# Optimization experiments

Hardware: AMD Instinct MI355X
Metric: run time of the kernel (lower is better)

The kernel has to match this reference:

```python
import jax, jax.numpy as jnp
import numpy as np
from jax import lax

T_LEN, BATCH, D_IN, D_HID, N_LAYERS = 512, 32, 512, 512, 4


def setup_inputs() -> dict:
    key = jax.random.key(0)
    kx, kw, ku = jax.random.split(key, 3)
    x = jax.random.normal(kx, (T_LEN, BATCH, D_IN), dtype=jnp.float32)
    # xavier-ish scale on input kernels to keep the relu recurrence stable
    W = jax.random.normal(kw, (N_LAYERS, D_HID, D_IN), dtype=jnp.float32) * (1.0 / np.sqrt(D_IN))
    b = jnp.zeros((N_LAYERS, D_HID), dtype=jnp.float32)
    # diagonal recurrent weights in [0,1) so |u|<=1 (non-exploding)
    u = jax.random.uniform(ku, (N_LAYERS, D_HID), dtype=jnp.float32)
    return {"x": x, "W": W, "b": b, "u": u}


def _indrnn_layer(x, W_l, b_l, u_l):
    # x: [T, B, Din]; precompute input projection as one big GEMM
    xh = jnp.einsum('tbd,hd->tbh', x, W_l) + b_l  # [T, B, Dh]
    h0 = jnp.zeros((x.shape[1], W_l.shape[0]), dtype=x.dtype)

    def step(h, xh_t):
        h_new = jax.nn.relu(xh_t + u_l * h)
        return h_new, h_new

    _, outs = lax.scan(step, h0, xh)
    return outs  # [T, B, Dh]


def reference(x, W, b, u):
    out = x
    for l in range(W.shape[0]):  # fixed small layer count
        out = _indrnn_layer(out, W[l], b[l], u[l])
    return out
```

## Files before the change

kernel.cpp:

```cpp
#include <hip/hip_runtime.h>
#include <hip/hip_bf16.h>

typedef short bf16x8 __attribute__((ext_vector_type(8)));
typedef float f32x4 __attribute__((ext_vector_type(4)));

#define T_LEN 512
#define BATCH 32
#define D 512
#define M_TOT (T_LEN * BATCH)
#define NLAYER 4

#define BM 128
#define BN 128
#define BK 64
#define NT (D / BK)
#define EP 72

#define RBM 128
#define RBN 64
#define RSLOT (RBM * BK + RBN * BK)
#define RSMEM_BYTES (3 * RSLOT * 2)
#define REP 40

#define CH 32
#define NCH (T_LEN / CH)

#define SBAR()                             \
    do {                                   \
        __builtin_amdgcn_s_barrier();      \
        __builtin_amdgcn_sched_barrier(0); \
    } while (0)
#define VMCNT(n)                                                   \
    do {                                                           \
        asm volatile("s_waitcnt vmcnt(" #n ")" ::: "memory");      \
        __builtin_amdgcn_sched_barrier(0);                         \
    } while (0)

__global__ __launch_bounds__(256) void convert_k(const float* __restrict__ W,
                                                 __hip_bfloat16* __restrict__ Wb) {
    const int i = (blockIdx.x * 256 + threadIdx.x) * 4;
    float4 v = *(const float4*)(W + i);
    __hip_bfloat16 h0 = __float2bfloat16(v.x);
    __hip_bfloat16 h1 = __float2bfloat16(v.y);
    __hip_bfloat16 h2 = __float2bfloat16(v.z);
    __hip_bfloat16 h3 = __float2bfloat16(v.w);
    ushort4 o;
    o.x = *(const unsigned short*)&h0;
    o.y = *(const unsigned short*)&h1;
    o.z = *(const unsigned short*)&h2;
    o.w = *(const unsigned short*)&h3;
    *(ushort4*)(Wb + i) = o;
}

__global__ __launch_bounds__(256) void gemm_l0(const float* __restrict__ Agf0,
                                               const __hip_bfloat16* __restrict__ Bt,
                                               const float* __restrict__ bias,
                                               __hip_bfloat16* __restrict__ Cb) {
    constexpr int K = D;
    constexpr int N = D;
    __shared__ __hip_bfloat16 smem[4 * BM * BK];
    __hip_bfloat16* const AsP[2] = {smem, smem + BM * BK};
    __hip_bfloat16* const BsP[2] = {smem + 2 * BM * BK, smem + 3 * BM * BK};

    const int tid  = threadIdx.x;
    const int wave = tid >> 6;
    const int lane = tid & 63;

    const int bid = blockIdx.x;
    const int xcd = bid & 7;
    const int jb  = bid >> 3;
    const int bm  = xcd * 16 + (jb >> 2);
    const int bn  = jb & 3;

    const int wm = (wave >> 1) * 64;
    const int wn = (wave & 1) * 64;

    const int srow = lane >> 3;
    const int scol = ((lane & 7) ^ srow) * 8;

    const float* Agf = Agf0 + (size_t)(bm * BM) * K;
    const __hip_bfloat16* Bg = Bt + (size_t)(bn * BN) * K;

    f32x4 acc[4][4] = {};
    float4 va[4][2];

#define STAGE_B0(buf, k0)                                                                            \
    do {                                                                                             \
        _Pragma("unroll") for (int jj = 0; jj < 4; ++jj) {                                           \
            const int rbase = (jj * 4 + wave) * 8;                                                   \
            __builtin_amdgcn_global_load_lds(                                                        \
                (const __attribute__((address_space(1))) void*)(Bg + (size_t)(rbase + srow) * K + (k0) + scol), \
                (__attribute__((address_space(3))) void*)(&BsP[buf][rbase * BK]), 16, 0, 0);         \
        }                                                                                            \
    } while (0)

#define LOAD_A0(k0)                                                                                  \
    do {                                                                                             \
        _Pragma("unroll") for (int jj = 0; jj < 4; ++jj) {                                           \
            const int rbase = (jj * 4 + wave) * 8;                                                   \
            const float* s = Agf + (size_t)(rbase + srow) * K + (k0) + scol;                         \
            va[jj][0] = *(const float4*)s;                                                           \
            va[jj][1] = *(const float4*)(s + 4);                                                     \
        }                                                                                            \
    } while (0)

#define WRITE_A0(buf)                                                                                \
    do {                                                                                             \
        _Pragma("unroll") for (int jj = 0; jj < 4; ++jj) {                                           \
            const int rbase = (jj * 4 + wave) * 8;                                                   \
            bf16x8 pk;                                                                               \
            _Pragma("unroll") for (int q = 0; q < 4; ++q) {                                          \
                __hip_bfloat16 t0 = __float2bfloat16(((const float*)&va[jj][0])[q]);                 \
                __hip_bfloat16 t1 = __float2bfloat16(((const float*)&va[jj][1])[q]);                 \
                pk[q]     = *(const short*)&t0;                                                      \
                pk[q + 4] = *(const short*)&t1;                                                      \
            }                                                                                        \
            *(bf16x8*)(&AsP[buf][(rbase + srow) * BK + (lane & 7) * 8]) = pk;                        \
        }                                                                                            \
    } while (0)

#define COMPUTE0(buf)                                                                                \
    do {                                                                                             \
        bf16x8 af[4][2], bv[4][2];                                                                   \
        const int fr = lane & 15;                                                                    \
        const int kq = lane >> 4;                                                                    \
        _Pragma("unroll") for (int mi = 0; mi < 4; ++mi) {                                           \
            const int r = wm + mi * 16 + fr;                                                         \
            _Pragma("unroll") for (int kh = 0; kh < 2; ++kh) {                                       \
                const int c = ((kh * 4 + kq) ^ (fr & 7)) * 8;                                        \
                af[mi][kh] = *(const bf16x8*)(&AsP[buf][r * BK + c]);                                \
            }                                                                                        \
        }                                                                                            \
        _Pragma("unroll") for (int ni = 0; ni < 4; ++ni) {                                           \
            const int r = wn + ni * 16 + fr;                                                         \
            _Pragma("unroll") for (int kh = 0; kh < 2; ++kh) {                                       \
                const int c = ((kh * 4 + kq) ^ (fr & 7)) * 8;                                        \
                bv[ni][kh] = *(const bf16x8*)(&BsP[buf][r * BK + c]);                                \
            }                                                                                        \
        }                                                                                            \
        _Pragma("unroll") for (int kh = 0; kh < 2; ++kh)                                             \
            _Pragma("unroll") for (int mi = 0; mi < 4; ++mi)                                         \
                _Pragma("unroll") for (int ni = 0; ni < 4; ++ni)                                     \
                    acc[mi][ni] = __builtin_amdgcn_mfma_f32_16x16x32_bf16(af[mi][kh], bv[ni][kh],    \
                                                                          acc[mi][ni], 0, 0, 0);    \
    } while (0)

    LOAD_A0(0);
    STAGE_B0(0, 0);
    WRITE_A0(0);
    __syncthreads();
    int cur = 0;
#pragma unroll
    for (int kt = 1; kt < NT; ++kt) {
        LOAD_A0(kt * BK);
        STAGE_B0(cur ^ 1, kt * BK);
        COMPUTE0(cur);
        WRITE_A0(cur ^ 1);
        __syncthreads();
        cur ^= 1;
    }
    COMPUTE0(cur);
    __syncthreads();

    {
        __hip_bfloat16* S = smem + wave * (64 * EP);
        const int cfr = lane & 15;
        const int cfq = lane >> 4;
        float bs[4];
#pragma unroll
        for (int ni = 0; ni < 4; ++ni) bs[ni] = bias[bn * BN + wn + ni * 16 + cfr];
#pragma unroll
        for (int mi = 0; mi < 4; ++mi)
#pragma unroll
            for (int ni = 0; ni < 4; ++ni)
#pragma unroll
                for (int r = 0; r < 4; ++r)
                    S[(mi * 16 + cfq * 4 + r) * EP + ni * 16 + cfr] =
                        __float2bfloat16(acc[mi][ni][r] + bs[ni]);
        const int rq = lane >> 3;
        const int cl = (lane & 7) * 8;
#pragma unroll
        for (int p = 0; p < 8; ++p) {
            const int lr = p * 8 + rq;
            bf16x8 v = *(const bf16x8*)(S + lr * EP + cl);
            *(bf16x8*)(&Cb[(size_t)(bm * BM + wm + lr) * N + bn * BN + wn + cl]) = v;
        }
    }
#undef STAGE_B0
#undef LOAD_A0
#undef WRITE_A0
#undef COMPUTE0
}

__global__ __launch_bounds__(256) void gemm_r3(const __hip_bfloat16* __restrict__ A,
                                               const __hip_bfloat16* __restrict__ Bt,
                                               const float* __restrict__ bias,
                                               __hip_bfloat16* __restrict__ Cb) {
    constexpr int K = D;
    constexpr int N = D;
    extern __shared__ __hip_bfloat16 smem[];

    const int tid  = threadIdx.x;
    const int wave = tid >> 6;
    const int lane = tid & 63;

    const int bid = blockIdx.x;
    const int xcd = bid & 7;
    const int jb  = bid >> 3;
    const int bm  = xcd * 16 + (jb >> 3);
    const int bn  = jb & 7;

    const int wm = (wave >> 1) * 64;
    const int wn = (wave & 1) * 32;

    const int srow = lane >> 3;
    const int scol = ((lane & 7) ^ srow) * 8;

    const __hip_bfloat16* Ag = A  + (size_t)(bm * RBM) * K;
    const __hip_bfloat16* Bg = Bt + (size_t)(bn * RBN) * K;

    f32x4 acc[4][2] = {};

#define STAGE(slot, k0)                                                                              \
    do {                                                                                             \
        __hip_bfloat16* const Asl = smem + (slot) * RSLOT;                                           \
        __hip_bfloat16* const Bsl = Asl + RBM * BK;                                                  \
        _Pragma("unroll") for (int jj = 0; jj < 4; ++jj) {                                           \
            const int rbase = (wave * 4 + jj) * 8;                                                   \
            __builtin_amdgcn_global_load_lds(                                                        \
                (const __attribute__((address_space(1))) void*)(Ag + (size_t)(rbase + srow) * K + (k0) + scol), \
                (__attribute__((address_space(3))) void*)(Asl + rbase * BK), 16, 0, 0);              \
        }                                                                                            \
        _Pragma("unroll") for (int jj = 0; jj < 2; ++jj) {                                           \
            const int rbase = (wave * 2 + jj) * 8;                                                   \
            __builtin_amdgcn_global_load_lds(                                                        \
                (const __attribute__((address_space(1))) void*)(Bg + (size_t)(rbase + srow) * K + (k0) + scol), \
                (__attribute__((address_space(3))) void*)(Bsl + rbase * BK), 16, 0, 0);              \
        }                                                                                            \
    } while (0)

#define COMPUTE(slot)                                                                                \
    do {                                                                                             \
        const __hip_bfloat16* const Asl = smem + (slot) * RSLOT;                                     \
        const __hip_bfloat16* const Bsl = Asl + RBM * BK;                                            \
        bf16x8 af[4][2], bv[2][2];                                                                   \
        const int fr = lane & 15;                                                                    \
        const int kq = lane >> 4;                                                                    \
        _Pragma("unroll") for (int mi = 0; mi < 4; ++mi) {                                           \
            const int r = wm + mi * 16 + fr;                                                         \
            _Pragma("unroll") for (int kh = 0; kh < 2; ++kh) {                                       \
                const int c = ((kh * 4 + kq) ^ (fr & 7)) * 8;                                        \
                af[mi][kh] = *(const bf16x8*)(&Asl[r * BK + c]);                                     \
            }                                                                                        \
        }                                                                                            \
        _Pragma("unroll") for (int ni = 0; ni < 2; ++ni) {                                           \
            const int r = wn + ni * 16 + fr;                                                         \
            _Pragma("unroll") for (int kh = 0; kh < 2; ++kh) {                                       \
                const int c = ((kh * 4 + kq) ^ (fr & 7)) * 8;                                        \
                bv[ni][kh] = *(const bf16x8*)(&Bsl[r * BK + c]);                                     \
            }                                                                                        \
        }                                                                                            \
        _Pragma("unroll") for (int kh = 0; kh < 2; ++kh)                                             \
            _Pragma("unroll") for (int mi = 0; mi < 4; ++mi)                                         \
                _Pragma("unroll") for (int ni = 0; ni < 2; ++ni)                                     \
                    acc[mi][ni] = __builtin_amdgcn_mfma_f32_16x16x32_bf16(af[mi][kh], bv[ni][kh],    \
                                                                          acc[mi][ni], 0, 0, 0);    \
    } while (0)

    STAGE(0, 0);
    STAGE(1, BK);
    VMCNT(6);
    SBAR();

#pragma unroll
    for (int t = 0; t < NT; ++t) {
        if (t + 2 < NT) STAGE((t + 2) % 3, (t + 2) * BK);
        COMPUTE(t % 3);
        if (t < NT - 1) {
            if (t + 2 < NT) {
                VMCNT(6);
            } else {
                VMCNT(0);
            }
            SBAR();
        }
    }
    __syncthreads();

    {
        __hip_bfloat16* S = smem + wave * (64 * REP);
        const int cfr = lane & 15;
        const int cfq = lane >> 4;
        float bs[2];
#pragma unroll
        for (int ni = 0; ni < 2; ++ni) bs[ni] = bias[bn * RBN + wn + ni * 16 + cfr];
#pragma unroll
        for (int mi = 0; mi < 4; ++mi)
#pragma unroll
            for (int ni = 0; ni < 2; ++ni)
#pragma unroll
                for (int r = 0; r < 4; ++r)
                    S[(mi * 16 + cfq * 4 + r) * REP + ni * 16 + cfr] =
                        __float2bfloat16(acc[mi][ni][r] + bs[ni]);
        const int rq = lane >> 2;
        const int cl = (lane & 3) * 8;
#pragma unroll
        for (int p = 0; p < 4; ++p) {
            const int lr = p * 16 + rq;
            bf16x8 v = *(const bf16x8*)(S + lr * REP + cl);
            *(bf16x8*)(&Cb[(size_t)(bm * RBM + wm + lr) * N + bn * RBN + wn + cl]) = v;
        }
    }
#undef STAGE
#undef COMPUTE
}

template <int MODE>
__global__ __launch_bounds__(512) void scan_k(const __hip_bfloat16* __restrict__ xh,
                                              const float* __restrict__ u,
                                              float* __restrict__ outf,
                                              __hip_bfloat16* __restrict__ outb) {
    __shared__ float4 md[NCH][32];
    const int i2  = threadIdx.x & 31;
    const int c   = threadIdx.x >> 5;
    const int idx = blockIdx.x * 64 + i2 * 2;
    const float u0 = u[idx & (D - 1)];
    const float u1 = u[(idx + 1) & (D - 1)];

    const __hip_bfloat16* p = xh + (size_t)c * CH * M_TOT + idx;
    unsigned int xv[CH];
#pragma unroll
    for (int t = 0; t < CH; ++t) xv[t] = *(const unsigned int*)(p + (size_t)t * M_TOT);

    float m0 = 0.f, d0 = 0.f, m1 = 0.f, d1 = 0.f;
#pragma unroll
    for (int t = 0; t < CH; ++t) {
        const float a0 = __uint_as_float(xv[t] << 16);
        const float a1 = __uint_as_float(xv[t] & 0xffff0000u);
        m0 = fmaxf(fmaf(u0, m0, a0), 0.f);
        d0 = fmaf(u0, d0, a0);
        m1 = fmaxf(fmaf(u1, m1, a1), 0.f);
        d1 = fmaf(u1, d1, a1);
    }
    md[c][i2] = make_float4(m0, d0, m1, d1);
    __syncthreads();

    float e0 = u0 * u0, e1 = u1 * u1;
    e0 *= e0; e0 *= e0; e0 *= e0; e0 *= e0;
    e1 *= e1; e1 *= e1; e1 *= e1; e1 *= e1;
    float h0 = 0.f, h1 = 0.f;
    for (int jj = 0; jj < c; ++jj) {
        const float4 v = md[jj][i2];
        h0 = fmaxf(v.x, fmaf(e0, h0, v.y));
        h1 = fmaxf(v.z, fmaf(e1, h1, v.w));
    }

    const size_t base = (size_t)c * CH * M_TOT + idx;
#pragma unroll
    for (int t = 0; t < CH; ++t) {
        const size_t off = base + (size_t)t * M_TOT;
        const float a0 = __uint_as_float(xv[t] << 16);
        const float a1 = __uint_as_float(xv[t] & 0xffff0000u);
        h0 = fmaxf(fmaf(u0, h0, a0), 0.f);
        h1 = fmaxf(fmaf(u1, h1, a1), 0.f);
        if (MODE & 1) *(float2*)(outf + off) = make_float2(h0, h1);
        if (MODE & 2) {
            __hip_bfloat16 b0 = __float2bfloat16(h0);
            __hip_bfloat16 b1 = __float2bfloat16(h1);
            unsigned int pk = (unsigned int)(*(unsigned short*)&b0) |
                              ((unsigned int)(*(unsigned short*)&b1) << 16);
            *(unsigned int*)(outb + off) = pk;
        }
    }
}

extern "C" void kernel_launch(void* const* d_in, const int* in_sizes, int n_in,
                              void* d_out, int out_size, void* d_ws, size_t ws_size,
                              hipStream_t stream) {
    const float* x = (const float*)d_in[0];
    const float* W = (const float*)d_in[1];
    const float* b = (const float*)d_in[2];
    const float* u = (const float*)d_in[3];
    float* out = (float*)d_out;

    __hip_bfloat16* Wb = (__hip_bfloat16*)d_ws;
    __hip_bfloat16* Ab = (__hip_bfloat16*)((char*)d_ws + (size_t)NLAYER * D * D * 2);
    __hip_bfloat16* Xh = Ab + (size_t)M_TOT * D;

    (void)hipFuncSetAttribute((const void*)gemm_r3,
                              hipFuncAttributeMaxDynamicSharedMemorySize, RSMEM_BYTES);

    convert_k<<<(NLAYER * D * D / 4) / 256, 256, 0, stream>>>(W, Wb);

    for (int l = 0; l < NLAYER; ++l) {
        if (l == 0) {
            gemm_l0<<<(M_TOT / BM) * (D / BN), 256, 0, stream>>>(x, Wb, b, Xh);
        } else {
            gemm_r3<<<(M_TOT / RBM) * (D / RBN), 256, RSMEM_BYTES, stream>>>(
                Ab, Wb + (size_t)l * D * D, b + (size_t)l * D, Xh);
        }
        if (l < NLAYER - 1) {
            scan_k<2><<<M_TOT / 64, 512, 0, stream>>>(Xh, u + (size_t)l * D, nullptr, Ab);
        } else {
            scan_k<1><<<M_TOT / 64, 512, 0, stream>>>(Xh, u + (size_t)l * D, out, nullptr);
        }
    }
}
```

Baseline: 116.2 us.

## Keep the weight tile resident in LDS with per-wave streamed A tiles

Replaces the 128x64 triple-buffered GEMM used for layers 1-3 with a 256x64-tile, 512-thread kernel. The block loads its full 64xK weight slice into LDS once. Each of the 8 waves then streams its own 32-row activation slice through a private double buffer, so the K-loop needs no block-wide barriers and sets MFMA priority around the math. The aim is to cut repeated weight loads and barrier stalls, at the cost of higher LDS use per block and lower occupancy.

```diff
diff --git a/kernel.cpp b/kernel.cpp
--- a/kernel.cpp
+++ b/kernel.cpp
@@ -16,11 +16,13 @@
 #define NT (D / BK)
 #define EP 72
 
-#define RBM 128
-#define RBN 64
-#define RSLOT (RBM * BK + RBN * BK)
-#define RSMEM_BYTES (3 * RSLOT * 2)
-#define REP 40
+#define QBN 64
+#define QWROWS 32
+#define QBM 256
+#define QB_ELEMS (QBN * D)
+#define QA_SLOT (QWROWS * BK)
+#define QSMEM_BYTES ((QB_ELEMS + 8 * 2 * QA_SLOT) * 2)
+#define QEP 72
 
 #define CH 32
 #define NCH (T_LEN / CH)
@@ -30,10 +32,15 @@
         __builtin_amdgcn_s_barrier();      \
         __builtin_amdgcn_sched_barrier(0); \
     } while (0)
-#define VMCNT(n)                                                   \
-    do {                                                           \
-        asm volatile("s_waitcnt vmcnt(" #n ")" ::: "memory");      \
-        __builtin_amdgcn_sched_barrier(0);                         \
+#define VMCNT(n)                                              \
+    do {                                                      \
+        asm volatile("s_waitcnt vmcnt(" #n ")" ::: "memory"); \
+        __builtin_amdgcn_sched_barrier(0);                    \
+    } while (0)
+#define LGKM0()                                               \
+    do {                                                      \
+        asm volatile("s_waitcnt lgkmcnt(0)" ::: "memory");    \
+        __builtin_amdgcn_sched_barrier(0);                    \
     } while (0)
 
 __global__ __launch_bounds__(256) void convert_k(const float* __restrict__ W,
@@ -192,10 +199,10 @@
 #undef COMPUTE0
 }
 
-__global__ __launch_bounds__(256) void gemm_r3(const __hip_bfloat16* __restrict__ A,
-                                               const __hip_bfloat16* __restrict__ Bt,
-                                               const float* __restrict__ bias,
-                                               __hip_bfloat16* __restrict__ Cb) {
+__global__ __launch_bounds__(512) void gemm_resB(const __hip_bfloat16* __restrict__ A,
+                                                 const __hip_bfloat16* __restrict__ Bt,
+                                                 const float* __restrict__ bias,
+                                                 __hip_bfloat16* __restrict__ Cb) {
     constexpr int K = D;
     constexpr int N = D;
     extern __shared__ __hip_bfloat16 smem[];
@@ -207,112 +214,112 @@
     const int bid = blockIdx.x;
     const int xcd = bid & 7;
     const int jb  = bid >> 3;
-    const int bm  = xcd * 16 + (jb >> 3);
+    const int bm  = xcd * 8 + (jb >> 3);
     const int bn  = jb & 7;
 
-    const int wm = (wave >> 1) * 64;
-    const int wn = (wave & 1) * 32;
+    __hip_bfloat16* const Bsm = smem;
+    __hip_bfloat16* const Awv = smem + QB_ELEMS + wave * (2 * QA_SLOT);
 
     const int srow = lane >> 3;
-    const int scol = ((lane & 7) ^ srow) * 8;
-
-    const __hip_bfloat16* Ag = A  + (size_t)(bm * RBM) * K;
-    const __hip_bfloat16* Bg = Bt + (size_t)(bn * RBN) * K;
-
-    f32x4 acc[4][2] = {};
-
-#define STAGE(slot, k0)                                                                              \
+    const int sch  = lane & 7;
+
+    const __hip_bfloat16* Agw = A + (size_t)(bm * QBM + wave * QWROWS) * K;
+    const __hip_bfloat16* Bg  = Bt + (size_t)(bn * QBN) * K;
+
+    f32x4 acc[2][4] = {};
+
+#pragma unroll
+    for (int p = 0; p < 8; ++p) {
+        const int row = p * 8 + wave;
+        const int sc  = ((lane & ~7) | ((lane & 7) ^ (row & 7))) * 8;
+        __builtin_amdgcn_global_load_lds(
+            (const __attribute__((address_space(1))) void*)(Bg + (size_t)row * K + sc),
+            (__attribute__((address_space(3))) void*)(Bsm + row * D), 16, 0, 0);
+    }
+#define STAGE_A(slot, k0)                                                                            \
     do {                                                                                             \
-        __hip_bfloat16* const Asl = smem + (slot) * RSLOT;                                           \
-        __hip_bfloat16* const Bsl = Asl + RBM * BK;                                                  \
         _Pragma("unroll") for (int jj = 0; jj < 4; ++jj) {                                           \
-            const int rbase = (wave * 4 + jj) * 8;                                                   \
+            const int rbase = jj * 8;                                                                \
             __builtin_amdgcn_global_load_lds(                                                        \
-                (const __attribute__((address_space(1))) void*)(Ag + (size_t)(rbase + srow) * K + (k0) + scol), \
-                (__attribute__((address_space(3))) void*)(Asl + rbase * BK), 16, 0, 0);              \
-        }                                                                                            \
-        _Pragma("unroll") for (int jj = 0; jj < 2; ++jj) {                                           \
-            const int rbase = (wave * 2 + jj) * 8;                                                   \
-            __builtin_amdgcn_global_load_lds(                                                        \
-                (const __attribute__((address_space(1))) void*)(Bg + (size_t)(rbase + srow) * K + (k0) + scol), \
-                (__attribute__((address_space(3))) void*)(Bsl + rbase * BK), 16, 0, 0);              \
-        }                                                                                            \
-    } while (0)
-
-#define COMPUTE(slot)                                                                                \
-    do {                                                                                             \
-        const __hip_bfloat16* const Asl = smem + (slot) * RSLOT;                                     \
-        const __hip_bfloat16* const Bsl = Asl + RBM * BK;                                            \
-        bf16x8 af[4][2], bv[2][2];                                                                   \
-        const int fr = lane & 15;                                                                    \
-        const int kq = lane >> 4;                                                                    \
-        _Pragma("unroll") for (int mi = 0; mi < 4; ++mi) {                                           \
-            const int r = wm + mi * 16 + fr;                                                         \
-            _Pragma("unroll") for (int kh = 0; kh < 2; ++kh) {                                       \
-                const int c = ((kh * 4 + kq) ^ (fr & 7)) * 8;                                        \
-                af[mi][kh] = *(const bf16x8*)(&Asl[r * BK + c]);                                     \
-            }                                                                                        \
-        }                                                                                            \
-        _Pragma("unroll") for (int ni = 0; ni < 2; ++ni) {                                           \
-            const int r = wn + ni * 16 + fr;                                                         \
-            _Pragma("unroll") for (int kh = 0; kh < 2; ++kh) {                                       \
-                const int c = ((kh * 4 + kq) ^ (fr & 7)) * 8;                                        \
-                bv[ni][kh] = *(const bf16x8*)(&Bsl[r * BK + c]);                                     \
-            }                                                                                        \
-        }                                                                                            \
-        _Pragma("unroll") for (int kh = 0; kh < 2; ++kh)                                             \
-            _Pragma("unroll") for (int mi = 0; mi < 4; ++mi)                                         \
-                _Pragma("unroll") for (int ni = 0; ni < 2; ++ni)                                     \
-                    acc[mi][ni] = __builtin_amdgcn_mfma_f32_16x16x32_bf16(af[mi][kh], bv[ni][kh],    \
-                                                                          acc[mi][ni], 0, 0, 0);    \
-    } while (0)
-
-    STAGE(0, 0);
-    STAGE(1, BK);
-    VMCNT(6);
+                (const __attribute__((address_space(1))) void*)(Agw + (size_t)(rbase + srow) * K + (k0) + (sch ^ srow) * 8), \
+                (__attribute__((address_space(3))) void*)(Awv + (slot) * QA_SLOT + rbase * BK), 16, 0, 0); \
+        }                                                                                            \
+    } while (0)
+
+    STAGE_A(0, 0);
+    STAGE_A(1, BK);
+    VMCNT(4);
     SBAR();
 
+    const int fr = lane & 15;
+    const int kq = lane >> 4;
+
 #pragma unroll
     for (int t = 0; t < NT; ++t) {
-        if (t + 2 < NT) STAGE((t + 2) % 3, (t + 2) * BK);
-        COMPUTE(t % 3);
-        if (t < NT - 1) {
-            if (t + 2 < NT) {
-                VMCNT(6);
+        if (t > 0) {
+            if (t < NT - 1) {
+                VMCNT(4);
             } else {
                 VMCNT(0);
             }
-            SBAR();
-        }
-    }
-    __syncthreads();
+        }
+        const __hip_bfloat16* Asl = Awv + (t & 1) * QA_SLOT;
+        bf16x8 af[2][2], bv[4][2];
+#pragma unroll
+        for (int mi = 0; mi < 2; ++mi)
+#pragma unroll
+            for (int kh = 0; kh < 2; ++kh) {
+                const int c = ((kh * 4 + kq) ^ (fr & 7)) * 8;
+                af[mi][kh] = *(const bf16x8*)(&Asl[(mi * 16 + fr) * BK + c]);
+            }
+#pragma unroll
+        for (int ni = 0; ni < 4; ++ni)
+#pragma unroll
+            for (int kh = 0; kh < 2; ++kh) {
+                const int n = ni * 16 + fr;
+                const int c = t * BK + (((kh * 4 + kq) ^ (fr & 7)) * 8);
+                bv[ni][kh] = *(const bf16x8*)(&Bsm[n * D + c]);
+            }
+        LGKM0();
+        if (t + 2 < NT) STAGE_A(t & 1, (t + 2) * BK);
+        __builtin_amdgcn_sched_barrier(0);
+        __builtin_amdgcn_s_setprio(1);
+#pragma unroll
+        for (int kh = 0; kh < 2; ++kh)
+#pragma unroll
+            for (int mi = 0; mi < 2; ++mi)
+#pragma unroll
+                for (int ni = 0; ni < 4; ++ni)
+                    acc[mi][ni] = __builtin_amdgcn_mfma_f32_16x16x32_bf16(af[mi][kh], bv[ni][kh],
+                                                                          acc[mi][ni], 0, 0, 0);
+        __builtin_amdgcn_s_setprio(0);
+    }
+#undef STAGE_A
 
     {
-        __hip_bfloat16* S = smem + wave * (64 * REP);
+        __hip_bfloat16* S = Awv;
         const int cfr = lane & 15;
         const int cfq = lane >> 4;
-        float bs[2];
-#pragma unroll
-        for (int ni = 0; ni < 2; ++ni) bs[ni] = bias[bn * RBN + wn + ni * 16 + cfr];
-#pragma unroll
-        for (int mi = 0; mi < 4; ++mi)
-#pragma unroll
-            for (int ni = 0; ni < 2; ++ni)
+        float bs[4];
+#pragma unroll
+        for (int ni = 0; ni < 4; ++ni) bs[ni] = bias[bn * QBN + ni * 16 + cfr];
+#pragma unroll
+        for (int mi = 0; mi < 2; ++mi)
+#pragma unroll
+            for (int ni = 0; ni < 4; ++ni)
 #pragma unroll
                 for (int r = 0; r < 4; ++r)
-                    S[(mi * 16 + cfq * 4 + r) * REP + ni * 16 + cfr] =
+                    S[(mi * 16 + cfq * 4 + r) * QEP + ni * 16 + cfr] =
                         __float2bfloat16(acc[mi][ni][r] + bs[ni]);
-        const int rq = lane >> 2;
-        const int cl = (lane & 3) * 8;
+        const int rq = lane >> 3;
+        const int cl = (lane & 7) * 8;
 #pragma unroll
         for (int p = 0; p < 4; ++p) {
-            const int lr = p * 16 + rq;
-            bf16x8 v = *(const bf16x8*)(S + lr * REP + cl);
-            *(bf16x8*)(&Cb[(size_t)(bm * RBM + wm + lr) * N + bn * RBN + wn + cl]) = v;
-        }
-    }
-#undef STAGE
-#undef COMPUTE
+            const int lr = p * 8 + rq;
+            bf16x8 v = *(const bf16x8*)(S + lr * QEP + cl);
+            *(bf16x8*)(&Cb[(size_t)(bm * QBM + wave * QWROWS + lr) * N + bn * QBN + cl]) = v;
+        }
+    }
 }
 
 template <int MODE>
@@ -387,8 +394,8 @@
     __hip_bfloat16* Ab = (__hip_bfloat16*)((char*)d_ws + (size_t)NLAYER * D * D * 2);
     __hip_bfloat16* Xh = Ab + (size_t)M_TOT * D;
 
-    (void)hipFuncSetAttribute((const void*)gemm_r3,
-                              hipFuncAttributeMaxDynamicSharedMemorySize, RSMEM_BYTES);
+    (void)hipFuncSetAttribute((const void*)gemm_resB,
+                              hipFuncAttributeMaxDynamicSharedMemorySize, QSMEM_BYTES);
 
     convert_k<<<(NLAYER * D * D / 4) / 256, 256, 0, stream>>>(W, Wb);
 
@@ -396,7 +403,7 @@
         if (l == 0) {
             gemm_l0<<<(M_TOT / BM) * (D / BN), 256, 0, stream>>>(x, Wb, b, Xh);
         } else {
-            gemm_r3<<<(M_TOT / RBM) * (D / RBN), 256, RSMEM_BYTES, stream>>>(
+            gemm_resB<<<(M_TOT / QBM) * (D / QBN), 512, QSMEM_BYTES, stream>>>(
                 Ab, Wb + (size_t)l * D * D, b + (size_t)l * D, Xh);
         }
         if (l < NLAYER - 1) {
```

Result: faster. 113.6 us (-2.2%).
